# Optimization experiments

Measured on AMD Instinct MI355X. Metric: run time of the kernel, lower is better.

The kernel has to match this reference:

```python
import jax, jax.numpy as jnp
import numpy as np

NUM_HEADS = 8

def _gelu(x):
    return jax.nn.gelu(x, approximate=False)

def _ln(x, w, b, eps=1e-5):
    m = x.mean(-1, keepdims=True)
    v = ((x - m) ** 2).mean(-1, keepdims=True)
    return (x - m) / jnp.sqrt(v + eps) * w + b

def _conv(x, w, pad):
    return jax.lax.conv_general_dilated(x, w, (1, 1), [(pad, pad), (pad, pad)],
                                        dimension_numbers=('NCHW', 'OIHW', 'NCHW'))

def _dwconv(x, w):
    return jax.lax.conv_general_dilated(x, w, (1, 1), [(1, 1), (1, 1)],
                                        feature_group_count=x.shape[1],
                                        dimension_numbers=('NCHW', 'OIHW', 'NCHW'))

def setup_inputs():
    B, T, N, C, K = 4, 3, 4096, 256, 100
    ks = jax.random.split(jax.random.key(0), 16)
    p = lambda i, shape: (0.02 * jax.random.normal(ks[i], shape)).astype(jnp.float32)
    z = lambda n: jnp.zeros((n,), jnp.float32)
    return {
        'x': jax.random.normal(ks[0], (B, N, C), jnp.float32),
        'mem': jax.random.normal(ks[1], (B * T, N, C), jnp.float32),
        'conv1_w': p(2, (C, C, 7, 7)), 'conv1_b': z(C),
        'conv2_w': p(3, (C, C, 1, 1)), 'conv2_b': z(C),
        'conv3_w': p(4, (K, C, 1, 1)),
        'sim_alpha': jnp.ones((1,), jnp.float32), 'sim_beta': jnp.zeros((1,), jnp.float32),
        'ln_w': jnp.ones((C,), jnp.float32), 'ln_b': z(C),
        'q_w': p(5, (C, C)), 'q_b': z(C),
        'k_w': p(6, (C, C)), 'k_b': z(C),
        'v_w': p(7, (C, C)), 'v_b': z(C),
        'proj_w': p(8, (C, C)), 'proj_b': z(C),
        'fc1_w': p(9, (4 * C, C)), 'fc1_b': z(4 * C),
        'dw_w': p(10, (4 * C, 1, 3, 3)), 'dw_b': z(4 * C),
        'fc2_w': p(11, (C, 4 * C)), 'fc2_b': z(C),
        'H': 64, 'W': 64, 't': 3,
    }

def reference(x, mem, conv1_w, conv1_b, conv2_w, conv2_b, conv3_w, sim_alpha, sim_beta,
              ln_w, ln_b, q_w, q_b, k_w, k_b, v_w, v_b, proj_w, proj_b,
              fc1_w, fc1_b, dw_w, dw_b, fc2_w, fc2_b, H, W, t):
    B, N, C = x.shape
    T = t + 1
    # stack memory frames with current frame: [B, T, N, C]
    xt = jnp.concatenate([mem.reshape(B, t, N, C), x[:, None]], axis=1)
    img = xt.reshape(B * T, N, C).transpose(0, 2, 1).reshape(B * T, C, H, W)
    h = _gelu(_conv(img, conv1_w, 3) + conv1_b[:, None, None])
    h = _gelu(_conv(h, conv2_w, 0) + conv2_b[:, None, None])
    cz = _conv(h, conv3_w, 0)                      # [B*T, K, H, W]
    K = cz.shape[1]
    center = jax.nn.softmax(cz.reshape(B, T, K, N), axis=-1)
    center = jnp.einsum('btkn,btnc->btkc', center, xt)  # cluster centers [B,T,K,C]
    last, prev = center[:, -1], center[:, :-1]
    num = jnp.einsum('bkc,bskc->bsk', last, prev)
    den = jnp.maximum(jnp.linalg.norm(last, axis=-1)[:, None] * jnp.linalg.norm(prev, axis=-1), 1e-8)
    cos = jax.nn.sigmoid(sim_beta + sim_alpha * (num / den))  # [B, T-1, K]
    C_in = last + (cos[..., None] * prev).sum(axis=1)
    C_in = _ln(C_in, ln_w, ln_b)
    # cross-attention: queries = current frame tokens, keys/values = centers
    hd = C // NUM_HEADS
    q = (x @ q_w.T + q_b).reshape(B, N, NUM_HEADS, hd) * (hd ** -0.5)
    k = (C_in @ k_w.T + k_b).reshape(B, K, NUM_HEADS, hd)
    v = (C_in @ v_w.T + v_b).reshape(B, K, NUM_HEADS, hd)
    attn = jax.nn.softmax(jnp.einsum('bnhd,bkhd->bhnk', q, k), axis=-1)
    o = jnp.einsum('bhnk,bkhd->bnhd', attn, v).reshape(B, N, C)
    o = o @ proj_w.T + proj_b
    out = x + _ln(o, ln_w, ln_b)
    # MLP with depthwise conv
    y = out @ fc1_w.T + fc1_b                      # [B, N, 4C]
    yi = y.transpose(0, 2, 1).reshape(B, 4 * C, H, W)
    yi = _dwconv(yi, dw_w) + dw_b[:, None, None]
    y = _gelu(yi.reshape(B, 4 * C, N).transpose(0, 2, 1))
    y = y @ fc2_w.T + fc2_b
    return out + _ln(y, ln_w, ln_b)
```

## Files before the change

### kernel.cpp

```cpp
#include <hip/hip_runtime.h>
#include <math.h>

#define NN 4096
#define CC 256
#define HH 64
#define BT 16
#define KCC 100
#define NHH 8
#define HDD 32
#define C4 1024

typedef unsigned short bf16_t;
typedef short s16x8 __attribute__((ext_vector_type(8)));
typedef float f32x4 __attribute__((ext_vector_type(4)));
typedef float f32x16 __attribute__((ext_vector_type(16)));

__device__ __forceinline__ float bf2f(bf16_t h) {
  return __uint_as_float(((unsigned)h) << 16);
}
__device__ __forceinline__ bf16_t f2bf(float f) {
  unsigned u = __float_as_uint(f);
  return (bf16_t)((u + 0x7FFFu + ((u >> 16) & 1u)) >> 16);
}

__device__ __forceinline__ float gelu_f(float x) {
  return 0.5f * x * (1.0f + erff(x * 0.7071067811865475f));
}

__device__ __forceinline__ void g2l16(const void* g, void* l) {
  __builtin_amdgcn_global_load_lds((const __attribute__((address_space(1))) void*)g,
                                   (__attribute__((address_space(3))) void*)l, 16, 0, 0);
}

__device__ __forceinline__ float block_sum256(float v) {
  __shared__ float sh[4];
#pragma unroll
  for (int off = 32; off; off >>= 1) v += __shfl_xor(v, off, 64);
  __syncthreads();
  if ((threadIdx.x & 63) == 0) sh[threadIdx.x >> 6] = v;
  __syncthreads();
  return sh[0] + sh[1] + sh[2] + sh[3];
}

__device__ __forceinline__ const float* xt_base(const float* x, const float* mem, int bt) {
  int b = bt >> 2, tt = bt & 3;
  return (tt < 3) ? (mem + (size_t)(b * 3 + tt) * NN * CC)
                  : (x + (size_t)b * NN * CC);
}

__global__ __launch_bounds__(256) void prologue(const float* __restrict__ x,
                                                const float* __restrict__ mem,
                                                bf16_t* __restrict__ xtb,
                                                const float* __restrict__ w1,
                                                bf16_t* __restrict__ wtb,
                                                const float* __restrict__ c2w,
                                                const float* __restrict__ c3w,
                                                const float* __restrict__ qw,
                                                const float* __restrict__ pw,
                                                const float* __restrict__ f1w,
                                                const float* __restrict__ f2w,
                                                bf16_t* __restrict__ wbz) {
  int bid = blockIdx.x;
  int tid = threadIdx.x;
  if (bid < 16384) {
    int i = bid * 256 + tid;
    int c4 = i & 63;
    int n = (i >> 6) & 4095;
    int bt = i >> 18;
    const float* src = xt_base(x, mem, bt) + (size_t)n * CC + c4 * 4;
    float4 v = *(const float4*)src;
    ushort4 o;
    o.x = f2bf(v.x); o.y = f2bf(v.y); o.z = f2bf(v.z); o.w = f2bf(v.w);
    *(ushort4*)(xtb + (size_t)i * 4) = o;
  } else if (bid < 19520) {
    int i = (bid - 16384) * 256 + tid;
    int cj = i & 7;
    int t = i >> 3;
    int co = t & 63; t >>= 6;
    int oc = t & 3; t >>= 2;
    int kx = t % 7; t /= 7;
    int cq = t & 3; t >>= 2;
    int cg = t & 7;
    int ky = t >> 3;
    int ci = cg * 32 + oc * 8 + cj;
    int cog = cq * 64 + co;
    wtb[i] = f2bf(w1[((size_t)(cog * CC + ci) * 7 + ky) * 7 + kx]);
  } else {
    int j = (bid - 19520) * 256 + tid;
    float v;
    if (j < 65536) v = c2w[j];
    else if (j < 91136) v = c3w[j - 65536];
    else if (j < 156672) v = qw[j - 91136];
    else if (j < 222208) v = pw[j - 156672];
    else if (j < 484352) v = f1w[j - 222208];
    else v = f2w[j - 484352];
    wbz[j] = f2bf(v);
  }
}

__global__ __launch_bounds__(512, 4) void conv1_mfma(const bf16_t* __restrict__ xtb,
                                                     const bf16_t* __restrict__ wtb,
                                                     const float* __restrict__ bias,
                                                     bf16_t* __restrict__ h1) {
  int bid = blockIdx.x;
  int cq = bid & 3;
  int rem = bid >> 2;
  int bt = rem & 15;
  int rb = rem >> 4;
  int r0 = rb * 8;
  int co0 = cq * 64;
  int tid = threadIdx.x;
  int wv = tid >> 6;
  int lane = tid & 63;
  int l31 = lane & 31;
  int h = lane >> 5;
  __shared__ __align__(16) short As[14][2][70][8];
  __shared__ __align__(16) short Ws[2][7][2][64][8];
  {
    s16x8 z = {0, 0, 0, 0, 0, 0, 0, 0};
    for (int i = tid; i < 14 * 2 * 70; i += 512) *(s16x8*)((short*)As + i * 8) = z;
  }
  __syncthreads();
  f32x16 acc[2][2] = {};
  const bf16_t* xb = xtb + (size_t)bt * (NN * CC);
  for (int cig = 0; cig < 16; ++cig) {
    int ci0 = cig * 16;
    int cg = cig >> 1;
    int ob = (cig & 1) * 2;
    for (int t = wv; t < 28; t += 8) {
      int rr = t >> 1, go = t & 1;
      int r = r0 - 3 + rr;
      if (r >= 0 && r < HH) {
        const bf16_t* gsrc = xb + ((size_t)(r * 64 + lane)) * CC + ci0 + go * 8;
        g2l16(gsrc, &As[rr][go][3][0]);
      }
    }
    {
      const bf16_t* wk = wtb + ((size_t)((0 * 8 + cg) * 4 + cq)) * (1792 * 8);
      for (int t = wv; t < 14; t += 8) {
        int kx = t >> 1, go = t & 1;
        g2l16(wk + (size_t)(kx * 4 + ob + go) * 512 + lane * 8, &Ws[0][kx][go][0][0]);
      }
    }
    __syncthreads();
    for (int ky = 0; ky < 7; ++ky) {
      int cur = ky & 1;
      if (ky < 6) {
        const bf16_t* wk = wtb + ((size_t)(((ky + 1) * 8 + cg) * 4 + cq)) * (1792 * 8);
        for (int t = wv; t < 14; t += 8) {
          int kx = t >> 1, go = t & 1;
          g2l16(wk + (size_t)(kx * 4 + ob + go) * 512 + lane * 8,
                &Ws[cur ^ 1][kx][go][0][0]);
        }
      }
#pragma unroll
      for (int kx = 0; kx < 7; ++kx) {
        s16x8 fa[2], fb[2];
#pragma unroll
        for (int mt = 0; mt < 2; ++mt)
          fa[mt] = *(const s16x8*)&As[wv + ky][h][mt * 32 + l31 + kx][0];
#pragma unroll
        for (int nt = 0; nt < 2; ++nt)
          fb[nt] = *(const s16x8*)&Ws[cur][kx][h][nt * 32 + l31][0];
#pragma unroll
        for (int mt = 0; mt < 2; ++mt)
#pragma unroll
          for (int nt = 0; nt < 2; ++nt)
            acc[mt][nt] = __builtin_amdgcn_mfma_f32_32x32x16_bf16(
                fa[mt], fb[nt], acc[mt][nt], 0, 0, 0);
      }
      __syncthreads();
    }
  }
  int row = r0 + wv;
  const size_t xbase = (size_t)bt * (NN * CC);
#pragma unroll
  for (int nt = 0; nt < 2; ++nt) {
    int co = co0 + nt * 32 + l31;
    float bs = bias[co];
#pragma unroll
    for (int mt = 0; mt < 2; ++mt) {
#pragma unroll
      for (int rg = 0; rg < 16; ++rg) {
        int px = mt * 32 + (rg & 3) + 8 * (rg >> 2) + 4 * h;
        float vv = acc[mt][nt][rg] + bs;
        h1[xbase + (size_t)(row * 64 + px) * CC + co] = f2bf(gelu_f(vv));
      }
    }
  }
}

template <int GELU, int BIAS, int TOUT, int OBF>
__global__ __launch_bounds__(256) void gemm_mfma(const bf16_t* __restrict__ A,
                                                 const bf16_t* __restrict__ W,
                                                 const float* __restrict__ bias,
                                                 void* __restrict__ outp,
                                                 int M, int N, int K, int ldo,
                                                 size_t aStr, size_t oStr) {
  __shared__ short As[128][40];
  __shared__ short Bs[128][40];
  A += (size_t)blockIdx.z * aStr;
  size_t obase = (size_t)blockIdx.z * oStr;
  int tid = threadIdx.x;
  int n0 = blockIdx.x * 128, m0 = blockIdx.y * 128;
  int lane = tid & 63, wv = tid >> 6;
  int wm = wv & 1, wn = wv >> 1;
  int lm = lane & 15, g = lane >> 4;
  f32x4 acc[4][4] = {};
  int r1 = tid >> 2, kq = tid & 3;
  int r2 = r1 + 64;
  for (int k0 = 0; k0 < K; k0 += 32) {
    *(s16x8*)&As[r1][kq * 8] = *(const s16x8*)(A + (size_t)(m0 + r1) * K + k0 + kq * 8);
    *(s16x8*)&As[r2][kq * 8] = *(const s16x8*)(A + (size_t)(m0 + r2) * K + k0 + kq * 8);
    s16x8 z = {0, 0, 0, 0, 0, 0, 0, 0};
    s16x8 b1 = z, b2 = z;
    if (n0 + r1 < N) b1 = *(const s16x8*)(W + (size_t)(n0 + r1) * K + k0 + kq * 8);
    if (n0 + r2 < N) b2 = *(const s16x8*)(W + (size_t)(n0 + r2) * K + k0 + kq * 8);
    *(s16x8*)&Bs[r1][kq * 8] = b1;
    *(s16x8*)&Bs[r2][kq * 8] = b2;
    __syncthreads();
    s16x8 af[4], bf[4];
#pragma unroll
    for (int mt = 0; mt < 4; ++mt)
      af[mt] = *(const s16x8*)&As[wm * 64 + mt * 16 + lm][g * 8];
#pragma unroll
    for (int nt = 0; nt < 4; ++nt)
      bf[nt] = *(const s16x8*)&Bs[wn * 64 + nt * 16 + lm][g * 8];
#pragma unroll
    for (int mt = 0; mt < 4; ++mt)
#pragma unroll
      for (int nt = 0; nt < 4; ++nt)
        acc[mt][nt] = __builtin_amdgcn_mfma_f32_16x16x32_bf16(af[mt], bf[nt],
                                                              acc[mt][nt], 0, 0, 0);
    __syncthreads();
  }
#pragma unroll
  for (int nt = 0; nt < 4; ++nt) {
    int n = n0 + wn * 64 + nt * 16 + lm;
    if (n >= N) continue;
    float bs = BIAS ? bias[n] : 0.f;
#pragma unroll
    for (int mt = 0; mt < 4; ++mt) {
#pragma unroll
      for (int rg = 0; rg < 4; ++rg) {
        int m = m0 + wm * 64 + mt * 16 + g * 4 + rg;
        float v = acc[mt][nt][rg] + bs;
        if (GELU) v = gelu_f(v);
        size_t idx = obase + (TOUT ? ((size_t)n * ldo + m) : ((size_t)m * ldo + n));
        if (OBF)
          ((bf16_t*)outp)[idx] = f2bf(v);
        else
          ((float*)outp)[idx] = v;
      }
    }
  }
}

__global__ __launch_bounds__(256) void gemm_kv(const float* __restrict__ cin,
                                               const float* __restrict__ kw,
                                               const float* __restrict__ kbias,
                                               const float* __restrict__ vw,
                                               const float* __restrict__ vbias,
                                               float* __restrict__ kout,
                                               float* __restrict__ vout) {
  const float* Wm = blockIdx.z ? vw : kw;
  const float* bias = blockIdx.z ? vbias : kbias;
  float* outp = blockIdx.z ? vout : kout;
  const int M = 400, N = 256, K = 256;
  __shared__ float As[16][68];
  __shared__ float Ws[16][68];
  int tid = threadIdx.x;
  int n0 = blockIdx.x * 64, m0 = blockIdx.y * 64;
  int txn = tid & 15, tym = tid >> 4;
  int mi = tid >> 2, kq = (tid & 3) * 4;
  float acc[4][4] = {};
  for (int k0 = 0; k0 < K; k0 += 16) {
    float4 av = {0, 0, 0, 0}, wvv = {0, 0, 0, 0};
    if (m0 + mi < M) av = *(const float4*)&cin[(size_t)(m0 + mi) * K + k0 + kq];
    if (n0 + mi < N) wvv = *(const float4*)&Wm[(size_t)(n0 + mi) * K + k0 + kq];
    As[kq + 0][mi] = av.x; As[kq + 1][mi] = av.y; As[kq + 2][mi] = av.z; As[kq + 3][mi] = av.w;
    Ws[kq + 0][mi] = wvv.x; Ws[kq + 1][mi] = wvv.y; Ws[kq + 2][mi] = wvv.z; Ws[kq + 3][mi] = wvv.w;
    __syncthreads();
#pragma unroll
    for (int ki = 0; ki < 16; ++ki) {
      float4 a4 = *(const float4*)&As[ki][tym * 4];
      float4 w4 = *(const float4*)&Ws[ki][txn * 4];
      float am[4] = {a4.x, a4.y, a4.z, a4.w};
      float wn[4] = {w4.x, w4.y, w4.z, w4.w};
#pragma unroll
      for (int i = 0; i < 4; ++i)
#pragma unroll
        for (int j = 0; j < 4; ++j) acc[i][j] += am[i] * wn[j];
    }
    __syncthreads();
  }
#pragma unroll
  for (int i = 0; i < 4; ++i) {
    int m = m0 + tym * 4 + i;
    if (m >= M) continue;
#pragma unroll
    for (int j = 0; j < 4; ++j) {
      int n = n0 + txn * 4 + j;
      outp[(size_t)m * 256 + n] = acc[i][j] + bias[n];
    }
  }
}

__global__ __launch_bounds__(256) void softmax_rows(bf16_t* __restrict__ p) {
  __shared__ float sh[8];
  int tid = threadIdx.x;
  bf16_t* base = p + (size_t)blockIdx.x * NN + tid * 16;
  s16x8 a = *(const s16x8*)base;
  s16x8 b = *(const s16x8*)(base + 8);
  float vals[16];
#pragma unroll
  for (int j = 0; j < 8; ++j) {
    vals[j] = bf2f((bf16_t)a[j]);
    vals[8 + j] = bf2f((bf16_t)b[j]);
  }
  float mx = -1e30f;
#pragma unroll
  for (int j = 0; j < 16; ++j) mx = fmaxf(mx, vals[j]);
#pragma unroll
  for (int off = 32; off; off >>= 1) mx = fmaxf(mx, __shfl_xor(mx, off, 64));
  if ((tid & 63) == 0) sh[tid >> 6] = mx;
  __syncthreads();
  mx = fmaxf(fmaxf(sh[0], sh[1]), fmaxf(sh[2], sh[3]));
  float s = 0.f;
#pragma unroll
  for (int j = 0; j < 16; ++j) {
    vals[j] = expf(vals[j] - mx);
    s += vals[j];
  }
#pragma unroll
  for (int off = 32; off; off >>= 1) s += __shfl_xor(s, off, 64);
  if ((tid & 63) == 0) sh[4 + (tid >> 6)] = s;
  __syncthreads();
  s = sh[4] + sh[5] + sh[6] + sh[7];
  float inv = 1.f / s;
  s16x8 oa, ob;
#pragma unroll
  for (int j = 0; j < 8; ++j) {
    oa[j] = (short)f2bf(vals[j] * inv);
    ob[j] = (short)f2bf(vals[8 + j] * inv);
  }
  *(s16x8*)base = oa;
  *(s16x8*)(base + 8) = ob;
}

__global__ __launch_bounds__(256) void center_mfma(const bf16_t* __restrict__ soft,
                                                   const bf16_t* __restrict__ xtb,
                                                   float* __restrict__ partial) {
  int c0 = blockIdx.x * 128;
  int bt = blockIdx.y;
  int nc = blockIdx.z;
  int tid = threadIdx.x;
  int lane = tid & 63, wv = tid >> 6;
  int wm = wv & 1, wn = wv >> 1;
  int lm = lane & 15, g = lane >> 4;
  __shared__ short As[128][40];
  __shared__ short Bs[128][40];
  f32x4 acc[4][4] = {};
  int r1 = tid >> 2, kq = tid & 3;
  int r2 = r1 + 64;
  int bk = tid & 31, bc = (tid >> 5) * 16;
  const bf16_t* sb = soft + (size_t)bt * NN + (size_t)nc * 512;
  const bf16_t* xb = xtb + ((size_t)bt * NN + (size_t)nc * 512) * CC + c0;
  for (int k0 = 0; k0 < 512; k0 += 32) {
    *(s16x8*)&As[r1][kq * 8] =
        *(const s16x8*)(sb + (size_t)r1 * (BT * NN) + k0 + kq * 8);
    if (r2 < KCC)
      *(s16x8*)&As[r2][kq * 8] =
          *(const s16x8*)(sb + (size_t)r2 * (BT * NN) + k0 + kq * 8);
    s16x8 v0 = *(const s16x8*)(xb + (size_t)(k0 + bk) * CC + bc);
    s16x8 v1 = *(const s16x8*)(xb + (size_t)(k0 + bk) * CC + bc + 8);
#pragma unroll
    for (int j = 0; j < 8; ++j) Bs[bc + j][bk] = v0[j];
#pragma unroll
    for (int j = 0; j < 8; ++j) Bs[bc + 8 + j][bk] = v1[j];
    __syncthreads();
    s16x8 af[4], bf[4];
#pragma unroll
    for (int mt = 0; mt < 4; ++mt)
      af[mt] = *(const s16x8*)&As[wm * 64 + mt * 16 + lm][g * 8];
#pragma unroll
    for (int nt = 0; nt < 4; ++nt)
      bf[nt] = *(const s16x8*)&Bs[wn * 64 + nt * 16 + lm][g * 8];
#pragma unroll
    for (int mt = 0; mt < 4; ++mt)
#pragma unroll
      for (int nt = 0; nt < 4; ++nt)
        acc[mt][nt] = __builtin_amdgcn_mfma_f32_16x16x32_bf16(af[mt], bf[nt],
                                                              acc[mt][nt], 0, 0, 0);
    __syncthreads();
  }
  size_t obase = ((size_t)nc * BT + bt) * (KCC * CC);
#pragma unroll
  for (int nt = 0; nt < 4; ++nt) {
    int c = c0 + wn * 64 + nt * 16 + lm;
#pragma unroll
    for (int mt = 0; mt < 4; ++mt) {
#pragma unroll
      for (int rg = 0; rg < 4; ++rg) {
        int m = wm * 64 + mt * 16 + g * 4 + rg;
        if (m < KCC) partial[obase + (size_t)m * CC + c] = acc[mt][nt][rg];
      }
    }
  }
}

__global__ __launch_bounds__(256) void sim_cin(const float* __restrict__ partial,
                                               const float* __restrict__ alpha_p,
                                               const float* __restrict__ beta_p,
                                               const float* __restrict__ lnw,
                                               const float* __restrict__ lnb,
                                               float* __restrict__ cin) {
  int b = blockIdx.x / KCC, kc = blockIdx.x % KCC;
  int c = threadIdx.x;
  float p0 = 0.f, p1 = 0.f, p2 = 0.f, lst = 0.f;
#pragma unroll
  for (int nc = 0; nc < 8; ++nc) {
    size_t base = ((size_t)nc * BT) * KCC * CC;
    p0 += partial[base + ((size_t)(b * 4 + 0) * KCC + kc) * CC + c];
    p1 += partial[base + ((size_t)(b * 4 + 1) * KCC + kc) * CC + c];
    p2 += partial[base + ((size_t)(b * 4 + 2) * KCC + kc) * CC + c];
    lst += partial[base + ((size_t)(b * 4 + 3) * KCC + kc) * CC + c];
  }
  float ll = block_sum256(lst * lst);
  float q0 = block_sum256(p0 * p0);
  float q1 = block_sum256(p1 * p1);
  float q2 = block_sum256(p2 * p2);
  float d0 = block_sum256(lst * p0);
  float d1 = block_sum256(lst * p1);
  float d2 = block_sum256(lst * p2);
  float alpha = alpha_p[0], beta = beta_p[0];
  float nl = sqrtf(ll);
  float c0 = 1.f / (1.f + expf(-(beta + alpha * (d0 / fmaxf(nl * sqrtf(q0), 1e-8f)))));
  float c1 = 1.f / (1.f + expf(-(beta + alpha * (d1 / fmaxf(nl * sqrtf(q1), 1e-8f)))));
  float c2 = 1.f / (1.f + expf(-(beta + alpha * (d2 / fmaxf(nl * sqrtf(q2), 1e-8f)))));
  float v = lst + c0 * p0 + c1 * p1 + c2 * p2;
  float m = block_sum256(v) * (1.f / CC);
  float dv = v - m;
  float var = block_sum256(dv * dv) * (1.f / CC);
  cin[((size_t)b * KCC + kc) * CC + c] = dv * rsqrtf(var + 1e-5f) * lnw[c] + lnb[c];
}

__global__ __launch_bounds__(256) void attn2(const float* __restrict__ q,
                                             const float* __restrict__ kb,
                                             const float* __restrict__ vb,
                                             bf16_t* __restrict__ ob) {
  int b = blockIdx.y;
  int n0 = blockIdx.x * 8;
  int tid = threadIdx.x;
  __shared__ float qs[8][256];
  __shared__ float Ks[32][257];
  __shared__ float sc[8][8][104];
#pragma unroll
  for (int r = 0; r < 8; ++r)
    qs[r][tid] = q[((size_t)b * NN + n0 + r) * CC + tid] * 0.17677669529663687f;
  int nn = tid >> 5, kcl = tid & 31;
  for (int kt = 0; kt < 4; ++kt) {
    int kbase = kt * 32;
    int rows = (kbase + 32 <= KCC) ? 32 : (KCC - kbase);
    __syncthreads();
    for (int idx = tid; idx < rows * 256; idx += 256) {
      int rr = idx >> 8, cc = idx & 255;
      Ks[rr][cc] = kb[((size_t)b * KCC + kbase + rr) * CC + cc];
    }
    __syncthreads();
    if (kcl < rows) {
#pragma unroll
      for (int h = 0; h < NHH; ++h) {
        float s = 0.f;
#pragma unroll
        for (int d = 0; d < HDD; ++d) s += qs[nn][h * HDD + d] * Ks[kcl][h * HDD + d];
        sc[nn][h][kbase + kcl] = s;
      }
    }
  }
  __syncthreads();
  {
    int tnn = tid >> 5, th = (tid >> 2) & 7, j = tid & 3;
    float mx = -1e30f;
    for (int kc = j * 25; kc < j * 25 + 25; ++kc) mx = fmaxf(mx, sc[tnn][th][kc]);
    mx = fmaxf(mx, __shfl_xor(mx, 1, 64));
    mx = fmaxf(mx, __shfl_xor(mx, 2, 64));
    float sm = 0.f;
    for (int kc = j * 25; kc < j * 25 + 25; ++kc) {
      float e = expf(sc[tnn][th][kc] - mx);
      sc[tnn][th][kc] = e;
      sm += e;
    }
    sm += __shfl_xor(sm, 1, 64);
    sm += __shfl_xor(sm, 2, 64);
    float inv = 1.f / sm;
    for (int kc = j * 25; kc < j * 25 + 25; ++kc) sc[tnn][th][kc] *= inv;
  }
  __syncthreads();
  float o[8] = {0, 0, 0, 0, 0, 0, 0, 0};
  int h = tid >> 5;
  for (int kc = 0; kc < KCC; ++kc) {
    float v = vb[((size_t)b * KCC + kc) * CC + tid];
#pragma unroll
    for (int r = 0; r < 8; ++r) o[r] += sc[r][h][kc] * v;
  }
#pragma unroll
  for (int r = 0; r < 8; ++r)
    ob[((size_t)b * NN + n0 + r) * CC + tid] = f2bf(o[r]);
}

template <int WB>
__global__ __launch_bounds__(256) void add_ln(const float* __restrict__ res,
                                              const float* __restrict__ y,
                                              const float* __restrict__ lnw,
                                              const float* __restrict__ lnb,
                                              float* __restrict__ dst,
                                              bf16_t* __restrict__ dst_b) {
  size_t row = blockIdx.x;
  int c = threadIdx.x;
  float v = y[row * CC + c];
  float m = block_sum256(v) * (1.f / CC);
  float dv = v - m;
  float var = block_sum256(dv * dv) * (1.f / CC);
  float o = res[row * CC + c] + dv * rsqrtf(var + 1e-5f) * lnw[c] + lnb[c];
  dst[row * CC + c] = o;
  if (WB) dst_b[row * CC + c] = f2bf(o);
}

__global__ __launch_bounds__(256) void dwconv_kernel(const bf16_t* __restrict__ y1,
                                                     const float* __restrict__ dww,
                                                     const float* __restrict__ dwb,
                                                     bf16_t* __restrict__ y2) {
  int b = blockIdx.x >> 12;
  int n = blockIdx.x & 4095;
  int h = n >> 6, w = n & 63;
  int c40 = threadIdx.x * 4;
  float wreg[4][9];
#pragma unroll
  for (int j = 0; j < 4; ++j)
#pragma unroll
    for (int t2 = 0; t2 < 9; ++t2) wreg[j][t2] = dww[(size_t)(c40 + j) * 9 + t2];
  float acc[4] = {0, 0, 0, 0};
#pragma unroll
  for (int dy = 0; dy < 3; ++dy) {
    int r = h + dy - 1;
    if (r < 0 || r >= HH) continue;
#pragma unroll
    for (int dx = 0; dx < 3; ++dx) {
      int cl = w + dx - 1;
      if (cl < 0 || cl >= 64) continue;
      ushort4 u = *(const ushort4*)(y1 + ((size_t)b * NN + r * 64 + cl) * C4 + c40);
      int t2 = dy * 3 + dx;
      acc[0] += bf2f(u.x) * wreg[0][t2];
      acc[1] += bf2f(u.y) * wreg[1][t2];
      acc[2] += bf2f(u.z) * wreg[2][t2];
      acc[3] += bf2f(u.w) * wreg[3][t2];
    }
  }
  ushort4 o;
  o.x = f2bf(gelu_f(acc[0] + dwb[c40 + 0]));
  o.y = f2bf(gelu_f(acc[1] + dwb[c40 + 1]));
  o.z = f2bf(gelu_f(acc[2] + dwb[c40 + 2]));
  o.w = f2bf(gelu_f(acc[3] + dwb[c40 + 3]));
  *(ushort4*)(y2 + ((size_t)b * NN + n) * C4 + c40) = o;
}

extern "C" void kernel_launch(void* const* d_in, const int* in_sizes, int n_in,
                              void* d_out, int out_size, void* d_ws, size_t ws_size,
                              hipStream_t stream) {
  const float* x = (const float*)d_in[0];
  const float* mem = (const float*)d_in[1];
  const float* conv1_w = (const float*)d_in[2];
  const float* conv1_b = (const float*)d_in[3];
  const float* conv2_w = (const float*)d_in[4];
  const float* conv2_b = (const float*)d_in[5];
  const float* conv3_w = (const float*)d_in[6];
  const float* sim_a = (const float*)d_in[7];
  const float* sim_b = (const float*)d_in[8];
  const float* ln_w = (const float*)d_in[9];
  const float* ln_b = (const float*)d_in[10];
  const float* q_w = (const float*)d_in[11];
  const float* q_b = (const float*)d_in[12];
  const float* k_w = (const float*)d_in[13];
  const float* k_b = (const float*)d_in[14];
  const float* v_w = (const float*)d_in[15];
  const float* v_b = (const float*)d_in[16];
  const float* proj_w = (const float*)d_in[17];
  const float* proj_b = (const float*)d_in[18];
  const float* fc1_w = (const float*)d_in[19];
  const float* fc1_b = (const float*)d_in[20];
  const float* dw_w = (const float*)d_in[21];
  const float* dw_b = (const float*)d_in[22];
  const float* fc2_w = (const float*)d_in[23];
  const float* fc2_b = (const float*)d_in[24];

  char* base = (char*)d_ws;
  bf16_t* xtb = (bf16_t*)(base);
  bf16_t* by1 = (bf16_t*)(base);
  bf16_t* bh1 = (bf16_t*)(base + 33554432);
  float* qb = (float*)(base + 33554432);
  float* outb = (float*)(base + 33554432);
  float* partial = (float*)(base + 50331648);
  float* pbuf = (float*)(base + 50331648);
  bf16_t* y2 = (bf16_t*)(base + 50331648);
  bf16_t* czt = (bf16_t*)(base + 67108864);
  bf16_t* obz = (bf16_t*)(base + 67108864);
  bf16_t* outb_b = (bf16_t*)(base + 67108864);
  bf16_t* wtb = (bf16_t*)(base + 80216064);
  bf16_t* h2c = (bf16_t*)(base + 80216064);
  bf16_t* wbz = (bf16_t*)(base + 96993280);
  float* cin = (float*)(base + 100124672);
  float* kb = (float*)(base + 100534272);
  float* vb = (float*)(base + 100943872);
  float* dout = (float*)d_out;

  bf16_t* conv2_wb = wbz;
  bf16_t* conv3_wb = wbz + 65536;
  bf16_t* q_wb = wbz + 91136;
  bf16_t* proj_wb = wbz + 156672;
  bf16_t* fc1_wb = wbz + 222208;
  bf16_t* fc2_wb = wbz + 484352;

  prologue<<<22436, 256, 0, stream>>>(x, mem, xtb, conv1_w, wtb, conv2_w, conv3_w,
                                      q_w, proj_w, fc1_w, fc2_w, wbz);
  conv1_mfma<<<512, 512, 0, stream>>>(xtb, wtb, conv1_b, bh1);
  for (int i = 0; i < 2; ++i) {
    gemm_mfma<1, 1, 0, 1><<<dim3(2, 256, 1), 256, 0, stream>>>(
        bh1 + (size_t)i * 32768 * CC, conv2_wb, conv2_b, h2c, 32768, 256, 256, 256, 0, 0);
    gemm_mfma<0, 0, 1, 1><<<dim3(1, 256, 1), 256, 0, stream>>>(
        h2c, conv3_wb, nullptr, czt + (size_t)i * 32768, 32768, 100, 256, 65536, 0, 0);
  }
  softmax_rows<<<1600, 256, 0, stream>>>(czt);
  center_mfma<<<dim3(2, 16, 8), 256, 0, stream>>>(czt, xtb, partial);
  sim_cin<<<400, 256, 0, stream>>>(partial, sim_a, sim_b, ln_w, ln_b, cin);
  gemm_mfma<0, 1, 0, 0><<<dim3(2, 32, 4), 256, 0, stream>>>(
      xtb + (size_t)3 * NN * CC, q_wb, q_b, qb, 4096, 256, 256, 256,
      (size_t)4 * NN * CC, (size_t)NN * CC);
  gemm_kv<<<dim3(4, 7, 2), 256, 0, stream>>>(cin, k_w, k_b, v_w, v_b, kb, vb);
  attn2<<<dim3(512, 4), 256, 0, stream>>>(qb, kb, vb, obz);
  gemm_mfma<0, 1, 0, 0><<<dim3(2, 128, 1), 256, 0, stream>>>(obz, proj_wb, proj_b, pbuf,
                                                             16384, 256, 256, 256, 0, 0);
  add_ln<1><<<16384, 256, 0, stream>>>(x, pbuf, ln_w, ln_b, outb, outb_b);
  gemm_mfma<0, 1, 0, 1><<<dim3(8, 128, 1), 256, 0, stream>>>(outb_b, fc1_wb, fc1_b, by1,
                                                             16384, 1024, 256, 1024, 0, 0);
  dwconv_kernel<<<16384, 256, 0, stream>>>(by1, dw_w, dw_b, y2);
  gemm_mfma<0, 1, 0, 0><<<dim3(2, 32, 4), 256, 0, stream>>>(
      y2, fc2_wb, fc2_b, dout, 4096, 256, 1024, 256,
      (size_t)NN * C4, (size_t)NN * CC);
  add_ln<0><<<16384, 256, 0, stream>>>(outb, dout, ln_w, ln_b, dout, nullptr);
}
```

Baseline: 868.8 us.

## Load conv1 weights directly into registers and double-buffer input tiles

New measurement: 905.9 us. 1.04x slower.

```diff
diff --git a/kernel.cpp b/kernel.cpp
--- a/kernel.cpp
+++ b/kernel.cpp
@@ -114,63 +114,68 @@
   int lane = tid & 63;
   int l31 = lane & 31;
   int h = lane >> 5;
-  __shared__ __align__(16) short As[14][2][70][8];
-  __shared__ __align__(16) short Ws[2][7][2][64][8];
+  __shared__ __align__(16) short As[2][14][2][70][8];
   {
     s16x8 z = {0, 0, 0, 0, 0, 0, 0, 0};
-    for (int i = tid; i < 14 * 2 * 70; i += 512) *(s16x8*)((short*)As + i * 8) = z;
+    for (int i = tid; i < 2 * 14 * 2 * 70; i += 512) *(s16x8*)((short*)As + i * 8) = z;
   }
   __syncthreads();
   f32x16 acc[2][2] = {};
   const bf16_t* xb = xtb + (size_t)bt * (NN * CC);
+  for (int t = wv; t < 28; t += 8) {
+    int rr = t >> 1, go = t & 1;
+    int r = r0 - 3 + rr;
+    if (r >= 0 && r < HH)
+      g2l16(xb + ((size_t)(r * 64 + lane)) * CC + go * 8, &As[0][rr][go][3][0]);
+  }
+  __syncthreads();
+  int buf = 0;
   for (int cig = 0; cig < 16; ++cig) {
-    int ci0 = cig * 16;
+    if (cig < 15) {
+      int ci0n = (cig + 1) * 16;
+      for (int t = wv; t < 28; t += 8) {
+        int rr = t >> 1, go = t & 1;
+        int r = r0 - 3 + rr;
+        if (r >= 0 && r < HH)
+          g2l16(xb + ((size_t)(r * 64 + lane)) * CC + ci0n + go * 8,
+                &As[buf ^ 1][rr][go][3][0]);
+      }
+    }
     int cg = cig >> 1;
     int ob = (cig & 1) * 2;
-    for (int t = wv; t < 28; t += 8) {
-      int rr = t >> 1, go = t & 1;
-      int r = r0 - 3 + rr;
-      if (r >= 0 && r < HH) {
-        const bf16_t* gsrc = xb + ((size_t)(r * 64 + lane)) * CC + ci0 + go * 8;
-        g2l16(gsrc, &As[rr][go][3][0]);
+    const bf16_t* wb = wtb + ((size_t)cg * 4 + cq) * 14336;
+    int lvar = (ob + h) * 512 + l31 * 8;
+    s16x8 fbv[2][2];
+#pragma unroll
+    for (int nt = 0; nt < 2; ++nt)
+      fbv[0][nt] = *(const s16x8*)(wb + lvar + nt * 256);
+#pragma unroll
+    for (int ky = 0; ky < 7; ++ky) {
+#pragma unroll
+      for (int kx = 0; kx < 7; ++kx) {
+        int t = ky * 7 + kx;
+        int p = t & 1;
+        if (t < 48) {
+          int t1 = t + 1, ky1 = t1 / 7, kx1 = t1 - ky1 * 7;
+#pragma unroll
+          for (int nt = 0; nt < 2; ++nt)
+            fbv[p ^ 1][nt] = *(const s16x8*)(wb + (size_t)ky1 * 458752 +
+                                             kx1 * 2048 + lvar + nt * 256);
+        }
+        s16x8 fa0 = *(const s16x8*)&As[buf][wv + ky][h][l31 + kx][0];
+        s16x8 fa1 = *(const s16x8*)&As[buf][wv + ky][h][32 + l31 + kx][0];
+        acc[0][0] = __builtin_amdgcn_mfma_f32_32x32x16_bf16(fa0, fbv[p][0],
+                                                            acc[0][0], 0, 0, 0);
+        acc[0][1] = __builtin_amdgcn_mfma_f32_32x32x16_bf16(fa0, fbv[p][1],
+                                                            acc[0][1], 0, 0, 0);
+        acc[1][0] = __builtin_amdgcn_mfma_f32_32x32x16_bf16(fa1, fbv[p][0],
+                                                            acc[1][0], 0, 0, 0);
+        acc[1][1] = __builtin_amdgcn_mfma_f32_32x32x16_bf16(fa1, fbv[p][1],
+                                                            acc[1][1], 0, 0, 0);
       }
     }
-    {
-      const bf16_t* wk = wtb + ((size_t)((0 * 8 + cg) * 4 + cq)) * (1792 * 8);
-      for (int t = wv; t < 14; t += 8) {
-        int kx = t >> 1, go = t & 1;
-        g2l16(wk + (size_t)(kx * 4 + ob + go) * 512 + lane * 8, &Ws[0][kx][go][0][0]);
-      }
-    }
-    __syncthreads();
-    for (int ky = 0; ky < 7; ++ky) {
-      int cur = ky & 1;
-      if (ky < 6) {
-        const bf16_t* wk = wtb + ((size_t)(((ky + 1) * 8 + cg) * 4 + cq)) * (1792 * 8);
-        for (int t = wv; t < 14; t += 8) {
-          int kx = t >> 1, go = t & 1;
-          g2l16(wk + (size_t)(kx * 4 + ob + go) * 512 + lane * 8,
-                &Ws[cur ^ 1][kx][go][0][0]);
-        }
-      }
-#pragma unroll
-      for (int kx = 0; kx < 7; ++kx) {
-        s16x8 fa[2], fb[2];
-#pragma unroll
-        for (int mt = 0; mt < 2; ++mt)
-          fa[mt] = *(const s16x8*)&As[wv + ky][h][mt * 32 + l31 + kx][0];
-#pragma unroll
-        for (int nt = 0; nt < 2; ++nt)
-          fb[nt] = *(const s16x8*)&Ws[cur][kx][h][nt * 32 + l31][0];
-#pragma unroll
-        for (int mt = 0; mt < 2; ++mt)
-#pragma unroll
-          for (int nt = 0; nt < 2; ++nt)
-            acc[mt][nt] = __builtin_amdgcn_mfma_f32_32x32x16_bf16(
-                fa[mt], fb[nt], acc[mt][nt], 0, 0, 0);
-      }
-      __syncthreads();
-    }
+    __syncthreads();
+    buf ^= 1;
   }
   int row = r0 + wv;
   const size_t xbase = (size_t)bt * (NN * CC);
```
